# Kernel tuning notes

Hardware: AMD Instinct MI355X
Metric: run time of the kernel (lower is better)

Reference implementation:

```python
import jax, jax.numpy as jnp
import numpy as np

N_SENT = 262144
N_BAGS = 4096
HIDDEN = 256
HIER = 2
LAYER0 = 14
NUM_CLASSES = 53


def setup_inputs() -> dict:
    key = jax.random.key(0)
    ks = jax.random.split(key, 8)
    x = jax.random.normal(ks[0], (N_SENT, HIDDEN), dtype=jnp.float32)
    rel_emb0 = jax.random.normal(ks[1], (LAYER0, HIDDEN), dtype=jnp.float32) * 0.1
    rel_emb1 = jax.random.normal(ks[2], (NUM_CLASSES, HIDDEN), dtype=jnp.float32) * 0.1
    disc = jax.random.normal(ks[3], (NUM_CLASSES, 2 * HIDDEN), dtype=jnp.float32) * 0.05
    bias = jnp.zeros((NUM_CLASSES,), dtype=jnp.float32)
    # relation_levels[r] = (coarse node id, fine node id) for relation r
    relation_levels = jnp.stack(
        [jax.random.randint(ks[4], (NUM_CLASSES,), 0, LAYER0, dtype=jnp.int32),
         jnp.arange(NUM_CLASSES, dtype=jnp.int32)], axis=1)
    label_index = jax.random.randint(ks[5], (N_SENT,), 0, NUM_CLASSES, dtype=jnp.int32)
    # ragged bag boundaries: scope[0]=0, scope[-1]=N_SENT, interior sorted
    interior = jnp.sort(jax.random.randint(ks[6], (N_BAGS - 1,), 1, N_SENT, dtype=jnp.int32))
    scope = jnp.concatenate([jnp.zeros((1,), jnp.int32), interior,
                             jnp.full((1,), N_SENT, jnp.int32)])
    return {"x": x, "rel_emb0": rel_emb0, "rel_emb1": rel_emb1, "disc": disc,
            "bias": bias, "relation_levels": relation_levels,
            "label_index": label_index, "scope": scope}


def _segment_ids(scope, n):
    # scope: [B+1] sorted boundaries -> per-sentence bag id [n]
    marks = jnp.zeros((n,), jnp.int32).at[scope[1:-1]].add(1)
    return jnp.cumsum(marks)


def reference(x, rel_emb0, rel_emb1, disc, bias, relation_levels, label_index, scope):
    n = x.shape[0]
    b = scope.shape[0] - 1
    seg = _segment_ids(scope, n)                       # [N]
    ll = relation_levels[label_index]                  # [N, 2]
    # per-level attention logits: <rel_emb[level][node], x>
    lg0 = jnp.sum(rel_emb0[ll[:, 0]] * x, axis=-1)     # [N]
    lg1 = jnp.sum(rel_emb1[ll[:, 1]] * x, axis=-1)     # [N]
    logits = jnp.stack([lg0, lg1], axis=1)             # [N, hier]
    # ragged softmax per bag (stable)
    m = jax.ops.segment_max(logits, seg, num_segments=b)     # [B, hier]
    e = jnp.exp(logits - m[seg])
    s = jax.ops.segment_sum(e, seg, num_segments=b)          # [B, hier]
    score = e / s[seg]                                       # [N, hier]
    # attention-weighted sentence reduction per bag per level
    weighted = score[:, :, None] * x[:, None, :]             # [N, hier, H]
    repre = jax.ops.segment_sum(weighted, seg, num_segments=b)  # [B, hier, H]
    stack_repre = repre.reshape(b, HIER * HIDDEN)            # [B, 2H]
    return stack_repre @ disc.T + bias                       # [B, 53]
```

## Files before the change

### kernel.cpp

```cpp
#include <hip/hip_runtime.h>
#include <math.h>

#define HIDDEN 256
#define NUM_CLASSES 53
#define NWAVES 4
#define BLOCK (NWAVES * 64)
#define KP 8
#define COMB_BYTES (NUM_CLASSES * 2 * HIDDEN * 4)

template <int CTRL>
__device__ __forceinline__ float dpp_add(float v) {
    int t = __builtin_amdgcn_update_dpp(0, __float_as_int(v), CTRL, 0xf, 0xf, true);
    return v + __int_as_float(t);
}

__device__ __forceinline__ float wave_sum64(float v) {
    v = dpp_add<0x111>(v);
    v = dpp_add<0x112>(v);
    v = dpp_add<0x114>(v);
    v = dpp_add<0x118>(v);
    v = dpp_add<0x142>(v);
    v = dpp_add<0x143>(v);
    return __int_as_float(__builtin_amdgcn_readlane(__float_as_int(v), 63));
}

__global__ void build_comb_kernel(const float* __restrict__ rel_emb0,
                                  const float* __restrict__ rel_emb1,
                                  const int* __restrict__ relation_levels,
                                  float* __restrict__ comb) {
    const int c = blockIdx.x;
    const int t = threadIdx.x;
    const int2 rl = *reinterpret_cast<const int2*>(relation_levels + 2 * c);
    comb[c * 512 + t]       = rel_emb0[rl.x * HIDDEN + t];
    comb[c * 512 + 256 + t] = rel_emb1[rl.y * HIDDEN + t];
}

template <bool USE_COMB>
__global__ __launch_bounds__(BLOCK, 6) void hattn_fused_kernel(
    const float* __restrict__ x,
    const float* __restrict__ rel_emb0,
    const float* __restrict__ rel_emb1,
    const float* __restrict__ comb,
    const float* __restrict__ disc,
    const float* __restrict__ bias,
    const int* __restrict__ relation_levels,
    const int* __restrict__ label_index,
    const int* __restrict__ scope,
    float* __restrict__ out)
{
    const int bag   = blockIdx.x;
    const int start = __builtin_amdgcn_readfirstlane(scope[bag]);
    const int end   = __builtin_amdgcn_readfirstlane(scope[bag + 1]);

    const int tid  = threadIdx.x;
    const int lane = tid & 63;
    const int wave = tid >> 6;
    const int col  = lane << 2;

    float4 o0 = make_float4(0,0,0,0), o1 = make_float4(0,0,0,0);
    float  l0 = 0.f, l1 = 0.f;

    for (int rbase = start + wave * KP; rbase < end; rbase += NWAVES * KP) {
        const int rb = __builtin_amdgcn_readfirstlane(rbase);
        const int nv = end - rb;

        int lbl[KP];
        #pragma unroll
        for (int k = 0; k < KP; ++k) {
            const int rc = rb + ((k < nv) ? k : 0);
            lbl[k] = label_index[rc];
        }

        float4 xv[KP];
        #pragma unroll
        for (int k = 0; k < KP; ++k) {
            const int rc = rb + ((k < nv) ? k : 0);
            xv[k] = *reinterpret_cast<const float4*>(x + ((size_t)rc << 8) + col);
        }

        #pragma unroll
        for (int k = 0; k < KP; ++k) {
            float4 r0, r1;
            if constexpr (USE_COMB) {
                const float* cb = comb + ((size_t)lbl[k] << 9) + col;
                r0 = *reinterpret_cast<const float4*>(cb);
                r1 = *reinterpret_cast<const float4*>(cb + 256);
            } else {
                const int2 rl = *reinterpret_cast<const int2*>(relation_levels + 2 * lbl[k]);
                r0 = *reinterpret_cast<const float4*>(rel_emb0 + ((size_t)rl.x << 8) + col);
                r1 = *reinterpret_cast<const float4*>(rel_emb1 + ((size_t)rl.y << 8) + col);
            }
            float p0 = xv[k].x*r0.x + xv[k].y*r0.y + xv[k].z*r0.z + xv[k].w*r0.w;
            float p1 = xv[k].x*r1.x + xv[k].y*r1.y + xv[k].z*r1.z + xv[k].w*r1.w;
            const float s0 = wave_sum64(p0);
            const float s1 = wave_sum64(p1);
            const float e0 = (k < nv) ? __expf(s0) : 0.f;
            const float e1 = (k < nv) ? __expf(s1) : 0.f;
            l0 += e0;  l1 += e1;
            o0.x += e0*xv[k].x; o0.y += e0*xv[k].y; o0.z += e0*xv[k].z; o0.w += e0*xv[k].w;
            o1.x += e1*xv[k].x; o1.y += e1*xv[k].y; o1.z += e1*xv[k].z; o1.w += e1*xv[k].w;
        }
    }

    __shared__ alignas(16) float s_o[2][NWAVES][HIDDEN];
    __shared__ float s_l[NWAVES][2];
    __shared__ alignas(16) float s_repre[2 * HIDDEN];
    __shared__ float s_inv[2];

    *reinterpret_cast<float4*>(&s_o[0][wave][col]) = o0;
    *reinterpret_cast<float4*>(&s_o[1][wave][col]) = o1;
    if (lane == 0) { s_l[wave][0] = l0; s_l[wave][1] = l1; }
    __syncthreads();

    {
        const int t = tid;
        const float a0 = s_o[0][0][t] + s_o[0][1][t] + s_o[0][2][t] + s_o[0][3][t];
        const float a1 = s_o[1][0][t] + s_o[1][1][t] + s_o[1][2][t] + s_o[1][3][t];
        s_repre[t]          = a0;
        s_repre[HIDDEN + t] = a1;
        if (tid == 0) {
            const float L0 = s_l[0][0] + s_l[1][0] + s_l[2][0] + s_l[3][0];
            const float L1 = s_l[0][1] + s_l[1][1] + s_l[2][1] + s_l[3][1];
            s_inv[0] = (L0 > 0.f) ? 1.f / L0 : 0.f;
            s_inv[1] = (L1 > 0.f) ? 1.f / L1 : 0.f;
        }
    }
    __syncthreads();

    {
        const int c  = tid >> 2;
        const int l4 = tid & 3;
        if (c < NUM_CLASSES) {
            const float4* dr = reinterpret_cast<const float4*>(disc + (size_t)c * (2 * HIDDEN));
            const float4* rp = reinterpret_cast<const float4*>(s_repre);
            float pH0 = 0.f, pH1 = 0.f;
            #pragma unroll
            for (int i = 0; i < 16; ++i) {
                const int idx = l4 + 4 * i;
                const float4 a = rp[idx];
                const float4 d = dr[idx];
                pH0 += a.x*d.x + a.y*d.y + a.z*d.z + a.w*d.w;
            }
            #pragma unroll
            for (int i = 16; i < 32; ++i) {
                const int idx = l4 + 4 * i;
                const float4 a = rp[idx];
                const float4 d = dr[idx];
                pH1 += a.x*d.x + a.y*d.y + a.z*d.z + a.w*d.w;
            }
            float p = pH0 * s_inv[0] + pH1 * s_inv[1];
            p = dpp_add<0xB1>(p);
            p = dpp_add<0x4E>(p);
            if (l4 == 0) out[bag * NUM_CLASSES + c] = p + bias[c];
        }
    }
}

extern "C" void kernel_launch(void* const* d_in, const int* in_sizes, int n_in,
                              void* d_out, int out_size, void* d_ws, size_t ws_size,
                              hipStream_t stream) {
    const float* x               = (const float*)d_in[0];
    const float* rel_emb0        = (const float*)d_in[1];
    const float* rel_emb1        = (const float*)d_in[2];
    const float* disc            = (const float*)d_in[3];
    const float* bias            = (const float*)d_in[4];
    const int*   relation_levels = (const int*)d_in[5];
    const int*   label_index     = (const int*)d_in[6];
    const int*   scope           = (const int*)d_in[7];
    float*       out             = (float*)d_out;

    const int n_bags = in_sizes[7] - 1;

    if (d_ws != nullptr && ws_size >= (size_t)COMB_BYTES) {
        float* comb = (float*)d_ws;
        build_comb_kernel<<<NUM_CLASSES, HIDDEN, 0, stream>>>(
            rel_emb0, rel_emb1, relation_levels, comb);
        hattn_fused_kernel<true><<<n_bags, BLOCK, 0, stream>>>(
            x, rel_emb0, rel_emb1, comb, disc, bias,
            relation_levels, label_index, scope, out);
    } else {
        hattn_fused_kernel<false><<<n_bags, BLOCK, 0, stream>>>(
            x, rel_emb0, rel_emb1, nullptr, disc, bias,
            relation_levels, label_index, scope, out);
    }
}
```

Measured before the change: 466.0 us.

## Double-buffer sentence batch loads to overlap next-batch fetch with current compute

Restructures the per-wave sentence loop into a software pipeline with two register buffers, prefetching the next batch of x rows and labels while the current batch is reduced. The batch size drops from 8 to 4 rows per wave, and the launch-bounds occupancy hint goes from 6 to 4 to leave room for the extra registers. Embedding rows for a batch are now loaded together before the dot products. The goal is to hide global memory latency in this bandwidth-bound ragged reduction. The cost is higher register pressure and lower occupancy, which could offset the gain.

```diff
diff --git a/kernel.cpp b/kernel.cpp
--- a/kernel.cpp
+++ b/kernel.cpp
@@ -5,7 +5,8 @@
 #define NUM_CLASSES 53
 #define NWAVES 4
 #define BLOCK (NWAVES * 64)
-#define KP 8
+#define KP 4
+#define STRIDE (NWAVES * KP)
 #define COMB_BYTES (NUM_CLASSES * 2 * HIDDEN * 4)
 
 template <int CTRL>
@@ -36,7 +37,7 @@
 }
 
 template <bool USE_COMB>
-__global__ __launch_bounds__(BLOCK, 6) void hattn_fused_kernel(
+__global__ __launch_bounds__(BLOCK, 4) void hattn_fused_kernel(
     const float* __restrict__ x,
     const float* __restrict__ rel_emb0,
     const float* __restrict__ rel_emb1,
@@ -60,45 +61,66 @@
     float4 o0 = make_float4(0,0,0,0), o1 = make_float4(0,0,0,0);
     float  l0 = 0.f, l1 = 0.f;
 
-    for (int rbase = start + wave * KP; rbase < end; rbase += NWAVES * KP) {
-        const int rb = __builtin_amdgcn_readfirstlane(rbase);
-        const int nv = end - rb;
-
-        int lbl[KP];
+    auto load_batch = [&](int rbq, float4 (&xv)[KP], int (&lbl)[KP]) {
+        const int nvq = end - rbq;
         #pragma unroll
         for (int k = 0; k < KP; ++k) {
-            const int rc = rb + ((k < nv) ? k : 0);
+            const int rc = rbq + ((k < nvq) ? k : 0);
             lbl[k] = label_index[rc];
-        }
-
-        float4 xv[KP];
+            xv[k]  = *reinterpret_cast<const float4*>(x + ((size_t)rc << 8) + col);
+        }
+    };
+
+    auto process_batch = [&](int rbq, const float4 (&xv)[KP], const int (&lbl)[KP]) {
+        const int nvq = end - rbq;
+        float4 r0[KP], r1[KP];
         #pragma unroll
         for (int k = 0; k < KP; ++k) {
-            const int rc = rb + ((k < nv) ? k : 0);
-            xv[k] = *reinterpret_cast<const float4*>(x + ((size_t)rc << 8) + col);
-        }
-
+            if constexpr (USE_COMB) {
+                const float* cb = comb + ((size_t)lbl[k] << 9) + col;
+                r0[k] = *reinterpret_cast<const float4*>(cb);
+                r1[k] = *reinterpret_cast<const float4*>(cb + 256);
+            } else {
+                const int2 rl = *reinterpret_cast<const int2*>(relation_levels + 2 * lbl[k]);
+                r0[k] = *reinterpret_cast<const float4*>(rel_emb0 + ((size_t)rl.x << 8) + col);
+                r1[k] = *reinterpret_cast<const float4*>(rel_emb1 + ((size_t)rl.y << 8) + col);
+            }
+        }
         #pragma unroll
         for (int k = 0; k < KP; ++k) {
-            float4 r0, r1;
-            if constexpr (USE_COMB) {
-                const float* cb = comb + ((size_t)lbl[k] << 9) + col;
-                r0 = *reinterpret_cast<const float4*>(cb);
-                r1 = *reinterpret_cast<const float4*>(cb + 256);
-            } else {
-                const int2 rl = *reinterpret_cast<const int2*>(relation_levels + 2 * lbl[k]);
-                r0 = *reinterpret_cast<const float4*>(rel_emb0 + ((size_t)rl.x << 8) + col);
-                r1 = *reinterpret_cast<const float4*>(rel_emb1 + ((size_t)rl.y << 8) + col);
-            }
-            float p0 = xv[k].x*r0.x + xv[k].y*r0.y + xv[k].z*r0.z + xv[k].w*r0.w;
-            float p1 = xv[k].x*r1.x + xv[k].y*r1.y + xv[k].z*r1.z + xv[k].w*r1.w;
+            float p0 = xv[k].x*r0[k].x + xv[k].y*r0[k].y + xv[k].z*r0[k].z + xv[k].w*r0[k].w;
+            float p1 = xv[k].x*r1[k].x + xv[k].y*r1[k].y + xv[k].z*r1[k].z + xv[k].w*r1[k].w;
             const float s0 = wave_sum64(p0);
             const float s1 = wave_sum64(p1);
-            const float e0 = (k < nv) ? __expf(s0) : 0.f;
-            const float e1 = (k < nv) ? __expf(s1) : 0.f;
+            const float e0 = (k < nvq) ? __expf(s0) : 0.f;
+            const float e1 = (k < nvq) ? __expf(s1) : 0.f;
             l0 += e0;  l1 += e1;
             o0.x += e0*xv[k].x; o0.y += e0*xv[k].y; o0.z += e0*xv[k].z; o0.w += e0*xv[k].w;
             o1.x += e1*xv[k].x; o1.y += e1*xv[k].y; o1.z += e1*xv[k].z; o1.w += e1*xv[k].w;
+        }
+    };
+
+    {
+        int rb = start + wave * KP;
+        if (rb < end) {
+            float4 xvA[KP], xvB[KP];
+            int    lblA[KP], lblB[KP];
+            load_batch(rb, xvA, lblA);
+            for (;;) {
+                const int rbn = rb + STRIDE;
+                const bool hn = rbn < end;
+                if (hn) load_batch(rbn, xvB, lblB);
+                process_batch(rb, xvA, lblA);
+                if (!hn) break;
+                rb = rbn;
+
+                const int rbn2 = rb + STRIDE;
+                const bool hn2 = rbn2 < end;
+                if (hn2) load_batch(rbn2, xvA, lblA);
+                process_batch(rb, xvB, lblB);
+                if (!hn2) break;
+                rb = rbn2;
+            }
         }
     }
 
```

After: 407.2 us. 1.14x faster.

## Split each bag across multiple blocks with a separate partial-reduction final kernel

Applied to the files above, without the earlier changes.

Each bag is now processed by four blocks that each write partial weighted sums and exp totals to workspace, and a second kernel combines the partials, normalizes and applies the classifier. Per-wave row batches shrink from 8 to 4 and the occupancy hint rises. The aim is more parallelism and better load balance across ragged bags in a latency-bound kernel. The cost is an extra launch and partial-buffer traffic, and it needs a larger workspace or falls back to the single-kernel path.

```diff
diff --git a/kernel.cpp b/kernel.cpp
--- a/kernel.cpp
+++ b/kernel.cpp
@@ -5,8 +5,11 @@
 #define NUM_CLASSES 53
 #define NWAVES 4
 #define BLOCK (NWAVES * 64)
-#define KP 8
-#define COMB_BYTES (NUM_CLASSES * 2 * HIDDEN * 4)
+#define KP 4
+#define SPLIT 4
+#define PART_STRIDE 520
+#define COMB_FLOATS (NUM_CLASSES * 2 * HIDDEN)
+#define COMB_BYTES (COMB_FLOATS * 4)
 
 template <int CTRL>
 __device__ __forceinline__ float dpp_add(float v) {
@@ -35,12 +38,144 @@
     comb[c * 512 + 256 + t] = rel_emb1[rl.y * HIDDEN + t];
 }
 
-template <bool USE_COMB>
-__global__ __launch_bounds__(BLOCK, 6) void hattn_fused_kernel(
+__global__ __launch_bounds__(BLOCK, 8) void hattn_partial_kernel(
+    const float* __restrict__ x,
+    const float* __restrict__ comb,
+    const int* __restrict__ label_index,
+    const int* __restrict__ scope,
+    float* __restrict__ part)
+{
+    const int blk = blockIdx.x;
+    const int bag = blk >> 2;
+    const int j   = blk & (SPLIT - 1);
+    const int start = __builtin_amdgcn_readfirstlane(scope[bag]);
+    const int end   = __builtin_amdgcn_readfirstlane(scope[bag + 1]);
+
+    const int tid  = threadIdx.x;
+    const int lane = tid & 63;
+    const int wave = tid >> 6;
+    const int col  = lane << 2;
+    const int slot = j * NWAVES + wave;
+
+    float4 o0 = make_float4(0,0,0,0), o1 = make_float4(0,0,0,0);
+    float  l0 = 0.f, l1 = 0.f;
+
+    for (int rb0 = start + slot * KP; rb0 < end; rb0 += SPLIT * NWAVES * KP) {
+        const int rb = __builtin_amdgcn_readfirstlane(rb0);
+        const int nv = end - rb;
+
+        int    lbl[KP];
+        float4 xv[KP];
+        #pragma unroll
+        for (int k = 0; k < KP; ++k) {
+            const int rc = rb + ((k < nv) ? k : 0);
+            lbl[k] = label_index[rc];
+            xv[k]  = *reinterpret_cast<const float4*>(x + ((size_t)rc << 8) + col);
+        }
+
+        #pragma unroll
+        for (int k = 0; k < KP; ++k) {
+            const float* cb = comb + ((size_t)lbl[k] << 9) + col;
+            const float4 r0 = *reinterpret_cast<const float4*>(cb);
+            const float4 r1 = *reinterpret_cast<const float4*>(cb + 256);
+            float p0 = xv[k].x*r0.x + xv[k].y*r0.y + xv[k].z*r0.z + xv[k].w*r0.w;
+            float p1 = xv[k].x*r1.x + xv[k].y*r1.y + xv[k].z*r1.z + xv[k].w*r1.w;
+            const float s0 = wave_sum64(p0);
+            const float s1 = wave_sum64(p1);
+            const float e0 = (k < nv) ? __expf(s0) : 0.f;
+            const float e1 = (k < nv) ? __expf(s1) : 0.f;
+            l0 += e0;  l1 += e1;
+            o0.x += e0*xv[k].x; o0.y += e0*xv[k].y; o0.z += e0*xv[k].z; o0.w += e0*xv[k].w;
+            o1.x += e1*xv[k].x; o1.y += e1*xv[k].y; o1.z += e1*xv[k].z; o1.w += e1*xv[k].w;
+        }
+    }
+
+    __shared__ alignas(16) float s_o[2][NWAVES][HIDDEN];
+    __shared__ float s_l[NWAVES][2];
+
+    *reinterpret_cast<float4*>(&s_o[0][wave][col]) = o0;
+    *reinterpret_cast<float4*>(&s_o[1][wave][col]) = o1;
+    if (lane == 0) { s_l[wave][0] = l0; s_l[wave][1] = l1; }
+    __syncthreads();
+
+    float* pb = part + (size_t)blk * PART_STRIDE;
+    {
+        const int t = tid;
+        const float a0 = s_o[0][0][t] + s_o[0][1][t] + s_o[0][2][t] + s_o[0][3][t];
+        const float a1 = s_o[1][0][t] + s_o[1][1][t] + s_o[1][2][t] + s_o[1][3][t];
+        pb[t]          = a0;
+        pb[HIDDEN + t] = a1;
+        if (tid == 0) {
+            pb[512] = s_l[0][0] + s_l[1][0] + s_l[2][0] + s_l[3][0];
+            pb[513] = s_l[0][1] + s_l[1][1] + s_l[2][1] + s_l[3][1];
+        }
+    }
+}
+
+__global__ __launch_bounds__(BLOCK, 4) void hattn_final_kernel(
+    const float* __restrict__ part,
+    const float* __restrict__ disc,
+    const float* __restrict__ bias,
+    float* __restrict__ out)
+{
+    const int bag = blockIdx.x;
+    const int tid = threadIdx.x;
+
+    __shared__ alignas(16) float s_repre[2 * HIDDEN];
+    __shared__ float s_inv[2];
+
+    const float* pb = part + (size_t)bag * SPLIT * PART_STRIDE;
+    float a0 = 0.f, a1 = 0.f;
+    #pragma unroll
+    for (int j = 0; j < SPLIT; ++j) {
+        a0 += pb[j * PART_STRIDE + tid];
+        a1 += pb[j * PART_STRIDE + HIDDEN + tid];
+    }
+    s_repre[tid]          = a0;
+    s_repre[HIDDEN + tid] = a1;
+    if (tid == 0) {
+        float L0 = 0.f, L1 = 0.f;
+        #pragma unroll
+        for (int j = 0; j < SPLIT; ++j) {
+            L0 += pb[j * PART_STRIDE + 512];
+            L1 += pb[j * PART_STRIDE + 513];
+        }
+        s_inv[0] = (L0 > 0.f) ? 1.f / L0 : 0.f;
+        s_inv[1] = (L1 > 0.f) ? 1.f / L1 : 0.f;
+    }
+    __syncthreads();
+
+    const int c  = tid >> 2;
+    const int l4 = tid & 3;
+    if (c < NUM_CLASSES) {
+        const float4* dr = reinterpret_cast<const float4*>(disc + (size_t)c * (2 * HIDDEN));
+        const float4* rp = reinterpret_cast<const float4*>(s_repre);
+        float pH0 = 0.f, pH1 = 0.f;
+        #pragma unroll
+        for (int i = 0; i < 16; ++i) {
+            const int idx = l4 + 4 * i;
+            const float4 a = rp[idx];
+            const float4 d = dr[idx];
+            pH0 += a.x*d.x + a.y*d.y + a.z*d.z + a.w*d.w;
+        }
+        #pragma unroll
+        for (int i = 16; i < 32; ++i) {
+            const int idx = l4 + 4 * i;
+            const float4 a = rp[idx];
+            const float4 d = dr[idx];
+            pH1 += a.x*d.x + a.y*d.y + a.z*d.z + a.w*d.w;
+        }
+        float p = pH0 * s_inv[0] + pH1 * s_inv[1];
+        p = dpp_add<0xB1>(p);
+        p = dpp_add<0x4E>(p);
+        if (l4 == 0) out[bag * NUM_CLASSES + c] = p + bias[c];
+    }
+}
+
+__global__ __launch_bounds__(BLOCK, 4) void hattn_fused_kernel(
     const float* __restrict__ x,
     const float* __restrict__ rel_emb0,
     const float* __restrict__ rel_emb1,
-    const float* __restrict__ comb,
     const float* __restrict__ disc,
     const float* __restrict__ bias,
     const int* __restrict__ relation_levels,
@@ -60,36 +195,21 @@
     float4 o0 = make_float4(0,0,0,0), o1 = make_float4(0,0,0,0);
     float  l0 = 0.f, l1 = 0.f;
 
-    for (int rbase = start + wave * KP; rbase < end; rbase += NWAVES * KP) {
-        const int rb = __builtin_amdgcn_readfirstlane(rbase);
+    for (int rb0 = start + wave * KP; rb0 < end; rb0 += NWAVES * KP) {
+        const int rb = __builtin_amdgcn_readfirstlane(rb0);
         const int nv = end - rb;
-
-        int lbl[KP];
+        int lbl[KP]; float4 xv[KP];
         #pragma unroll
         for (int k = 0; k < KP; ++k) {
             const int rc = rb + ((k < nv) ? k : 0);
             lbl[k] = label_index[rc];
-        }
-
-        float4 xv[KP];
+            xv[k]  = *reinterpret_cast<const float4*>(x + ((size_t)rc << 8) + col);
+        }
         #pragma unroll
         for (int k = 0; k < KP; ++k) {
-            const int rc = rb + ((k < nv) ? k : 0);
-            xv[k] = *reinterpret_cast<const float4*>(x + ((size_t)rc << 8) + col);
-        }
-
-        #pragma unroll
-        for (int k = 0; k < KP; ++k) {
-            float4 r0, r1;
-            if constexpr (USE_COMB) {
-                const float* cb = comb + ((size_t)lbl[k] << 9) + col;
-                r0 = *reinterpret_cast<const float4*>(cb);
-                r1 = *reinterpret_cast<const float4*>(cb + 256);
-            } else {
-                const int2 rl = *reinterpret_cast<const int2*>(relation_levels + 2 * lbl[k]);
-                r0 = *reinterpret_cast<const float4*>(rel_emb0 + ((size_t)rl.x << 8) + col);
-                r1 = *reinterpret_cast<const float4*>(rel_emb1 + ((size_t)rl.y << 8) + col);
-            }
+            const int2 rl = *reinterpret_cast<const int2*>(relation_levels + 2 * lbl[k]);
+            const float4 r0 = *reinterpret_cast<const float4*>(rel_emb0 + ((size_t)rl.x << 8) + col);
+            const float4 r1 = *reinterpret_cast<const float4*>(rel_emb1 + ((size_t)rl.y << 8) + col);
             float p0 = xv[k].x*r0.x + xv[k].y*r0.y + xv[k].z*r0.z + xv[k].w*r0.w;
             float p1 = xv[k].x*r1.x + xv[k].y*r1.y + xv[k].z*r1.z + xv[k].w*r1.w;
             const float s0 = wave_sum64(p0);
@@ -114,10 +234,8 @@
 
     {
         const int t = tid;
-        const float a0 = s_o[0][0][t] + s_o[0][1][t] + s_o[0][2][t] + s_o[0][3][t];
-        const float a1 = s_o[1][0][t] + s_o[1][1][t] + s_o[1][2][t] + s_o[1][3][t];
-        s_repre[t]          = a0;
-        s_repre[HIDDEN + t] = a1;
+        s_repre[t]          = s_o[0][0][t] + s_o[0][1][t] + s_o[0][2][t] + s_o[0][3][t];
+        s_repre[HIDDEN + t] = s_o[1][0][t] + s_o[1][1][t] + s_o[1][2][t] + s_o[1][3][t];
         if (tid == 0) {
             const float L0 = s_l[0][0] + s_l[1][0] + s_l[2][0] + s_l[3][0];
             const float L1 = s_l[0][1] + s_l[1][1] + s_l[2][1] + s_l[3][1];
@@ -127,32 +245,28 @@
     }
     __syncthreads();
 
-    {
-        const int c  = tid >> 2;
-        const int l4 = tid & 3;
-        if (c < NUM_CLASSES) {
-            const float4* dr = reinterpret_cast<const float4*>(disc + (size_t)c * (2 * HIDDEN));
-            const float4* rp = reinterpret_cast<const float4*>(s_repre);
-            float pH0 = 0.f, pH1 = 0.f;
-            #pragma unroll
-            for (int i = 0; i < 16; ++i) {
-                const int idx = l4 + 4 * i;
-                const float4 a = rp[idx];
-                const float4 d = dr[idx];
-                pH0 += a.x*d.x + a.y*d.y + a.z*d.z + a.w*d.w;
-            }
-            #pragma unroll
-            for (int i = 16; i < 32; ++i) {
-                const int idx = l4 + 4 * i;
-                const float4 a = rp[idx];
-                const float4 d = dr[idx];
-                pH1 += a.x*d.x + a.y*d.y + a.z*d.z + a.w*d.w;
-            }
-            float p = pH0 * s_inv[0] + pH1 * s_inv[1];
-            p = dpp_add<0xB1>(p);
-            p = dpp_add<0x4E>(p);
-            if (l4 == 0) out[bag * NUM_CLASSES + c] = p + bias[c];
-        }
+    const int c  = tid >> 2;
+    const int l4 = tid & 3;
+    if (c < NUM_CLASSES) {
+        const float4* dr = reinterpret_cast<const float4*>(disc + (size_t)c * (2 * HIDDEN));
+        const float4* rp = reinterpret_cast<const float4*>(s_repre);
+        float pH0 = 0.f, pH1 = 0.f;
+        #pragma unroll
+        for (int i = 0; i < 16; ++i) {
+            const int idx = l4 + 4 * i;
+            const float4 a = rp[idx]; const float4 d = dr[idx];
+            pH0 += a.x*d.x + a.y*d.y + a.z*d.z + a.w*d.w;
+        }
+        #pragma unroll
+        for (int i = 16; i < 32; ++i) {
+            const int idx = l4 + 4 * i;
+            const float4 a = rp[idx]; const float4 d = dr[idx];
+            pH1 += a.x*d.x + a.y*d.y + a.z*d.z + a.w*d.w;
+        }
+        float p = pH0 * s_inv[0] + pH1 * s_inv[1];
+        p = dpp_add<0xB1>(p);
+        p = dpp_add<0x4E>(p);
+        if (l4 == 0) out[bag * NUM_CLASSES + c] = p + bias[c];
     }
 }
 
@@ -170,17 +284,20 @@
     float*       out             = (float*)d_out;
 
     const int n_bags = in_sizes[7] - 1;
-
-    if (d_ws != nullptr && ws_size >= (size_t)COMB_BYTES) {
+    const size_t part_bytes = (size_t)n_bags * SPLIT * PART_STRIDE * sizeof(float);
+
+    if (d_ws != nullptr && ws_size >= COMB_BYTES + part_bytes) {
         float* comb = (float*)d_ws;
+        float* part = comb + COMB_FLOATS;
         build_comb_kernel<<<NUM_CLASSES, HIDDEN, 0, stream>>>(
             rel_emb0, rel_emb1, relation_levels, comb);
-        hattn_fused_kernel<true><<<n_bags, BLOCK, 0, stream>>>(
-            x, rel_emb0, rel_emb1, comb, disc, bias,
+        hattn_partial_kernel<<<n_bags * SPLIT, BLOCK, 0, stream>>>(
+            x, comb, label_index, scope, part);
+        hattn_final_kernel<<<n_bags, BLOCK, 0, stream>>>(
+            part, disc, bias, out);
+    } else {
+        hattn_fused_kernel<<<n_bags, BLOCK, 0, stream>>>(
+            x, rel_emb0, rel_emb1, disc, bias,
             relation_levels, label_index, scope, out);
-    } else {
-        hattn_fused_kernel<false><<<n_bags, BLOCK, 0, stream>>>(
-            x, rel_emb0, rel_emb1, nullptr, disc, bias,
-            relation_levels, label_index, scope, out);
-    }
-}
+    }
+}
```

Result: faster. 424.2 us (-9.0%).
